# Optimization experiments

Measured on AMD Instinct MI355X. Metric: run time of the kernel, lower is better.

The kernel has to match this reference:

```python
import jax, jax.numpy as jnp
import numpy as np

N = 50000   # nodes
E = 800000  # edges (before self-loops)
B = 2       # extra batch dim
EPS = 1e-5  # BatchNorm eps


def _glorot(k, fi, fo):
    return jax.random.normal(k, (fi, fo), jnp.float32) * (1.0 / np.sqrt(fi))


def setup_inputs() -> dict:
    key = jax.random.key(0)
    ks = jax.random.split(key, 8)
    x = jax.random.normal(ks[0], (1, B, N, 216), jnp.float32)
    edge_index = jax.random.randint(ks[1], (2, E), 0, N, dtype=jnp.int64)
    return {
        "x": x,
        "W1": _glorot(ks[2], 216, 64), "b1": jnp.zeros((64,), jnp.float32),
        "g1": jnp.ones((64,), jnp.float32), "be1": jnp.zeros((64,), jnp.float32),
        "W2": _glorot(ks[3], 64, 8), "b2": jnp.zeros((8,), jnp.float32),
        "g2": jnp.ones((8,), jnp.float32), "be2": jnp.zeros((8,), jnp.float32),
        "W3": _glorot(ks[4], 8, 3), "b3": jnp.zeros((3,), jnp.float32),
        "edge_index": edge_index,
    }


def _gcn_norm(edge_index, n):
    # add self-loops, symmetric normalization D^-1/2 (A+I) D^-1/2
    loops = jnp.arange(n, dtype=edge_index.dtype)
    row = jnp.concatenate([edge_index[0], loops])
    col = jnp.concatenate([edge_index[1], loops])
    deg = jnp.zeros((n,), jnp.float32).at[col].add(1.0)
    dinv = jnp.where(deg > 0, jax.lax.rsqrt(deg), 0.0)
    norm = dinv[row] * dinv[col]  # [E+N]
    return row, col, norm


def _gcn(x, W, b, row, col, norm):
    # x: [1, B, N, Fin]; transform then propagate along node axis (-2)
    xw = jnp.einsum('ubnf,fo->ubno', x, W)
    msgs = xw[:, :, row, :] * norm[None, None, :, None]     # gather at sources
    out = jnp.zeros_like(xw).at[:, :, col, :].add(msgs)     # scatter to targets
    return out + b


def _bn(h, g, be):
    # h: [B, C, N]; batch statistics over (B, N) per channel (training mode)
    mean = h.mean(axis=(0, 2), keepdims=True)
    var = h.var(axis=(0, 2), keepdims=True)
    return (h - mean) * jax.lax.rsqrt(var + EPS) * g[None, :, None] + be[None, :, None]


def reference(x, W1, b1, g1, be1, W2, b2, g2, be2, W3, b3, edge_index):
    n = x.shape[-2]
    row, col, norm = _gcn_norm(edge_index, n)

    h = jax.nn.relu(_gcn(x, W1, b1, row, col, norm))        # [1,B,N,64]
    h = jnp.swapaxes(h[0], 1, 2)                            # [B,64,N]
    h = _bn(h, g1, be1)
    h = jnp.swapaxes(h, 1, 2)[None]                         # [1,B,N,64]

    x1 = _gcn(h, W2, b2, row, col, norm)                    # [1,B,N,8]
    x2 = jax.nn.relu(x1)
    x2 = jnp.swapaxes(x2[0], 1, 2)                          # [B,8,N]
    x2 = _bn(x2, g2, be2)
    x2 = jnp.swapaxes(x2, 1, 2)[None]                       # [1,B,N,8]

    out = _gcn(x2, W3, b3, row, col, norm)                  # [1,B,N,3]
    return (out, x1)
```

## Files before the change

kernel.cpp:

```cpp
#include <hip/hip_runtime.h>
#include <stdint.h>

#define N_NODES 50000
#define N_EDGES 800000
#define BB 2
#define F0 216
#define ROWS (BB*N_NODES)
#define BN_EPS 1e-5f
#define NSB 49


__global__ void k_count(const int* __restrict__ ei, int* __restrict__ cnt) {
    int e = blockIdx.x*blockDim.x + threadIdx.x;
    if (e < N_EDGES) {
        int c = ei[N_EDGES + e];
        atomicAdd(&cnt[c], 1);
    }
}

__global__ void k_dinv(const int* __restrict__ cnt, float* __restrict__ dinv) {
    int i = blockIdx.x*blockDim.x + threadIdx.x;
    if (i < N_NODES) dinv[i] = rsqrtf((float)(cnt[i] + 1));
}

__global__ void k_scanA(const int* __restrict__ cnt, int* __restrict__ incl, int* __restrict__ part) {
    __shared__ int s[1024];
    int t = threadIdx.x;
    int i = blockIdx.x*1024 + t;
    s[t] = (i < N_NODES) ? cnt[i] : 0;
    __syncthreads();
    for (int off=1; off<1024; off<<=1) {
        int a = (t >= off) ? s[t-off] : 0;
        __syncthreads();
        s[t] += a;
        __syncthreads();
    }
    if (i < N_NODES) incl[i] = s[t];
    if (t == 1023) part[blockIdx.x] = s[t];
}

__global__ void k_scanB(int* part) {
    if (threadIdx.x == 0 && blockIdx.x == 0) {
        int run = 0;
        for (int b=0; b<NSB; b++) { int v = part[b]; part[b] = run; run += v; }
    }
}

__global__ void k_scanC(const int* __restrict__ cnt, const int* __restrict__ incl, const int* __restrict__ part,
                        int* __restrict__ offs, int* __restrict__ cursor) {
    int i = blockIdx.x*1024 + threadIdx.x;
    if (i < N_NODES) {
        int inc = part[blockIdx.x] + incl[i];
        int ex = inc - cnt[i];
        offs[i] = ex; cursor[i] = ex;
        if (i == N_NODES-1) offs[N_NODES] = inc;
    }
}

__global__ void k_fill(const int* __restrict__ ei, const float* __restrict__ dinv,
                       int* __restrict__ cursor, int* __restrict__ csr_src, float* __restrict__ csr_w) {
    int e = blockIdx.x*blockDim.x + threadIdx.x;
    if (e < N_EDGES) {
        int r = ei[e];
        int c = ei[N_EDGES + e];
        int slot = atomicAdd(&cursor[c], 1);
        csr_src[slot] = r;
        csr_w[slot]  = dinv[r];
    }
}

#define KC 24
__global__ __launch_bounds__(256,2) void k_gemm1(const float* __restrict__ x, const float* __restrict__ W1,
                                                 float* __restrict__ xw) {
    __shared__ float xs[F0*64];
    int t = threadIdx.x;
    int row0 = blockIdx.x * 64;

    int r  = t & 63;
    int kg = t >> 6;
    bool rowok = (row0 + r) < ROWS;
    const float* xr = x + (size_t)(row0 + r) * F0;
    for (int kb = 0; kb < F0; kb += 16) {
        int k0 = kb + kg*4;
        if (k0 < F0) {
            float4 v; v.x=v.y=v.z=v.w=0.f;
            if (rowok) v = *reinterpret_cast<const float4*>(xr + k0);
            xs[(k0+0)*64 + r] = v.x;
            xs[(k0+1)*64 + r] = v.y;
            xs[(k0+2)*64 + r] = v.z;
            xs[(k0+3)*64 + r] = v.w;
        }
    }
    __syncthreads();

    int o2 = t & 31;
    int rg = t >> 5;
    float acc0[8], acc1[8];
    #pragma unroll
    for (int j=0;j<8;j++){ acc0[j]=0.f; acc1[j]=0.f; }

    for (int kc = 0; kc < F0; kc += KC) {
        float wa[KC], wb[KC];
        #pragma unroll
        for (int kk=0; kk<KC; kk++) {
            wa[kk] = W1[(kc+kk)*64 + o2];
            wb[kk] = W1[(kc+kk)*64 + o2 + 32];
        }
        #pragma unroll
        for (int kk=0; kk<KC; kk++) {
            const float* xk = xs + (kc+kk)*64 + rg*8;
            float4 x0 = *reinterpret_cast<const float4*>(xk);
            float4 x1 = *reinterpret_cast<const float4*>(xk + 4);
            float w0 = wa[kk], w1 = wb[kk];
            acc0[0] += x0.x*w0; acc0[1] += x0.y*w0; acc0[2] += x0.z*w0; acc0[3] += x0.w*w0;
            acc0[4] += x1.x*w0; acc0[5] += x1.y*w0; acc0[6] += x1.z*w0; acc0[7] += x1.w*w0;
            acc1[0] += x0.x*w1; acc1[1] += x0.y*w1; acc1[2] += x0.z*w1; acc1[3] += x0.w*w1;
            acc1[4] += x1.x*w1; acc1[5] += x1.y*w1; acc1[6] += x1.z*w1; acc1[7] += x1.w*w1;
        }
    }

    #pragma unroll
    for (int j=0;j<8;j++) {
        int grow = row0 + rg*8 + j;
        if (grow < ROWS) {
            xw[(size_t)grow*64 + o2]      = acc0[j];
            xw[(size_t)grow*64 + o2 + 32] = acc1[j];
        }
    }
}

__global__ __launch_bounds__(256) void k_prop1(const float* __restrict__ xw, const int* __restrict__ offs,
                       const int* __restrict__ csr_src, const float* __restrict__ csr_w,
                       const float* __restrict__ dinv, const float* __restrict__ b1,
                       float* __restrict__ h, float* __restrict__ stat) {
    __shared__ float lsum[64], lsq[64];
    int t = threadIdx.x;
    if (t < 64) { lsum[t]=0.f; lsq[t]=0.f; }
    __syncthreads();
    int f = t & 63;
    int wid = blockIdx.x*4 + (t>>6);
    int nwaves = gridDim.x*4;
    float bias = b1[f];
    float ls=0.f, lq=0.f;
    for (int d = wid; d < N_NODES; d += nwaves) {
        int s0 = offs[d], s1 = offs[d+1];
        float a0=0.f, a1=0.f, p0=0.f, p1=0.f, q0=0.f, q1=0.f, r0=0.f, r1=0.f;
        int e = s0;
        for (; e+4 <= s1; e += 4) {
            int i0=csr_src[e], i1=csr_src[e+1], i2=csr_src[e+2], i3=csr_src[e+3];
            float w0=csr_w[e], w1=csr_w[e+1], w2=csr_w[e+2], w3=csr_w[e+3];
            a0 += w0*xw[(size_t)i0*64+f];  a1 += w0*xw[(size_t)(N_NODES+i0)*64+f];
            p0 += w1*xw[(size_t)i1*64+f];  p1 += w1*xw[(size_t)(N_NODES+i1)*64+f];
            q0 += w2*xw[(size_t)i2*64+f];  q1 += w2*xw[(size_t)(N_NODES+i2)*64+f];
            r0 += w3*xw[(size_t)i3*64+f];  r1 += w3*xw[(size_t)(N_NODES+i3)*64+f];
        }
        for (; e < s1; e++) {
            int src = csr_src[e]; float w = csr_w[e];
            a0 += w*xw[(size_t)src*64+f];  a1 += w*xw[(size_t)(N_NODES+src)*64+f];
        }
        a0 += p0 + q0 + r0;
        a1 += p1 + q1 + r1;
        float sd = dinv[d];
        a0 += sd * xw[(size_t)d*64 + f];
        a1 += sd * xw[(size_t)(N_NODES+d)*64 + f];
        float h0 = fmaxf(sd*a0 + bias, 0.f);
        float h1 = fmaxf(sd*a1 + bias, 0.f);
        h[(size_t)d*64 + f] = h0;
        h[(size_t)(N_NODES+d)*64 + f] = h1;
        ls += h0 + h1;
        lq += h0*h0 + h1*h1;
    }
    atomicAdd(&lsum[f], ls);
    atomicAdd(&lsq[f], lq);
    __syncthreads();
    if (t < 64) {
        atomicAdd(&stat[t],     lsum[t]);
        atomicAdd(&stat[64+t],  lsq[t]);
    }
}

__global__ void k_bnfin(const float* __restrict__ stat, const float* __restrict__ g,
                        const float* __restrict__ be, float* __restrict__ sc, int C) {
    int f = threadIdx.x;
    if (f < C) {
        float inv_n = 1.0f / (float)(BB*N_NODES);
        float mean = stat[f]*inv_n;
        float var  = stat[C+f]*inv_n - mean*mean;
        float is   = rsqrtf(var + BN_EPS);
        float scale = g[f]*is;
        sc[f]   = scale;
        sc[C+f] = be[f] - mean*scale;
    }
}

__global__ __launch_bounds__(256) void k_bn1_gemm2(const float* __restrict__ h, const float* __restrict__ sc1,
                        const float* __restrict__ W2, float* __restrict__ t2) {
    __shared__ float hs[32][68];
    __shared__ float w2s[64*8];
    int t = threadIdx.x;
    for (int i=t; i<512; i+=256) w2s[i] = W2[i];
    int row0 = blockIdx.x*32;
    for (int idx=t; idx<2048; idx+=256) {
        int r = idx>>6, f = idx&63;
        int grow = row0 + r;
        hs[r][f] = (grow < ROWS) ? h[(size_t)grow*64+f]*sc1[f] + sc1[64+f] : 0.f;
    }
    __syncthreads();
    int r = t >> 3, o = t & 7;
    float acc = 0.f;
    #pragma unroll
    for (int f=0; f<64; f++) acc += hs[r][f] * w2s[f*8+o];
    int grow = row0 + r;
    if (grow < ROWS) t2[(size_t)grow*8 + o] = acc;
}

__global__ __launch_bounds__(256) void k_prop2(const float* __restrict__ t2, const int* __restrict__ offs,
                       const int* __restrict__ csr_src, const float* __restrict__ csr_w,
                       const float* __restrict__ dinv, const float* __restrict__ b2,
                       float* __restrict__ x1_out, float* __restrict__ stat) {
    __shared__ float lsum[8], lsq[8];
    int t = threadIdx.x;
    if (t < 8) { lsum[t]=0.f; lsq[t]=0.f; }
    __syncthreads();
    int lane = t & 63;
    int o = lane & 7, b = (lane>>3)&1, es = lane>>4;
    int wid = blockIdx.x*4 + (t>>6);
    int nwaves = gridDim.x*4;
    float bias = b2[o];
    float ls=0.f, lq=0.f;
    for (int d=wid; d<N_NODES; d+=nwaves) {
        int s0=offs[d], s1=offs[d+1];
        float accA=0.f, accB=0.f;
        int e = s0 + es;
        for (; e+4 < s1; e += 8) {
            accA += csr_w[e]   * t2[(size_t)(b*N_NODES+csr_src[e])*8 + o];
            accB += csr_w[e+4] * t2[(size_t)(b*N_NODES+csr_src[e+4])*8 + o];
        }
        if (e < s1) accA += csr_w[e] * t2[(size_t)(b*N_NODES+csr_src[e])*8 + o];
        float acc = accA + accB;
        acc += __shfl_xor(acc, 16, 64);
        acc += __shfl_xor(acc, 32, 64);
        float sd = dinv[d];
        float val = sd*(acc + sd*t2[(size_t)(b*N_NODES+d)*8 + o]) + bias;
        if (es == 0) {
            x1_out[(size_t)(b*N_NODES+d)*8 + o] = val;
            float rv = fmaxf(val, 0.f);
            ls += rv; lq += rv*rv;
        }
    }
    if (es == 0) { atomicAdd(&lsum[o], ls); atomicAdd(&lsq[o], lq); }
    __syncthreads();
    if (t < 8) { atomicAdd(&stat[t], lsum[t]); atomicAdd(&stat[8+t], lsq[t]); }
}

__global__ void k_bn2_gemm3(const float* __restrict__ x1, const float* __restrict__ sc2,
                            const float* __restrict__ W3, float* __restrict__ t3) {
    int rowi = blockIdx.x*blockDim.x + threadIdx.x;
    if (rowi < ROWS) {
        float v[8];
        #pragma unroll
        for (int o=0;o<8;o++) {
            float r = fmaxf(x1[(size_t)rowi*8+o], 0.f);
            v[o] = r*sc2[o] + sc2[8+o];
        }
        #pragma unroll
        for (int c=0;c<3;c++) {
            float acc=0.f;
            #pragma unroll
            for (int o=0;o<8;o++) acc += v[o]*W3[o*3+c];
            t3[(size_t)rowi*4+c] = acc;
        }
        t3[(size_t)rowi*4+3] = 0.f;
    }
}

__global__ __launch_bounds__(256) void k_prop3(const float* __restrict__ t3, const int* __restrict__ offs,
                       const int* __restrict__ csr_src, const float* __restrict__ csr_w,
                       const float* __restrict__ dinv, const float* __restrict__ b3,
                       float* __restrict__ outp) {
    int t = threadIdx.x;
    int lane = t & 63;
    int c = lane & 3, b = (lane>>2)&1, es = lane>>3;
    int wid = blockIdx.x*4 + (t>>6);
    int nwaves = gridDim.x*4;
    float bias = (c<3) ? b3[c] : 0.f;
    for (int d=wid; d<N_NODES; d+=nwaves) {
        int s0=offs[d], s1=offs[d+1];
        float accA=0.f, accB=0.f;
        int e = s0 + es;
        for (; e+8 < s1; e += 16) {
            accA += csr_w[e]   * t3[(size_t)(b*N_NODES+csr_src[e])*4 + c];
            accB += csr_w[e+8] * t3[(size_t)(b*N_NODES+csr_src[e+8])*4 + c];
        }
        if (e < s1) accA += csr_w[e] * t3[(size_t)(b*N_NODES+csr_src[e])*4 + c];
        float acc = accA + accB;
        acc += __shfl_xor(acc, 8, 64);
        acc += __shfl_xor(acc, 16, 64);
        acc += __shfl_xor(acc, 32, 64);
        float sd = dinv[d];
        float val = sd*(acc + sd*t3[(size_t)(b*N_NODES+d)*4 + c]) + bias;
        if (es == 0 && c < 3) outp[(size_t)(b*N_NODES+d)*3 + c] = val;
    }
}

static inline size_t align256(size_t x){ return (x + 255) & ~(size_t)255; }

extern "C" void kernel_launch(void* const* d_in, const int* in_sizes, int n_in,
                              void* d_out, int out_size, void* d_ws, size_t ws_size,
                              hipStream_t stream) {
    const float* x   = (const float*)d_in[0];
    const float* W1  = (const float*)d_in[1];
    const float* b1  = (const float*)d_in[2];
    const float* g1  = (const float*)d_in[3];
    const float* be1 = (const float*)d_in[4];
    const float* W2  = (const float*)d_in[5];
    const float* b2  = (const float*)d_in[6];
    const float* g2  = (const float*)d_in[7];
    const float* be2 = (const float*)d_in[8];
    const float* W3  = (const float*)d_in[9];
    const float* b3  = (const float*)d_in[10];
    const int*   ei  = (const int*)d_in[11];

    float* outp   = (float*)d_out;
    float* x1_out = (float*)d_out + BB*N_NODES*3;

    char* w = (char*)d_ws;
    size_t off = 0;
    auto alloc = [&](size_t bytes) { void* p = w + off; off = align256(off + bytes); return p; };
    int*   cnt    = (int*)  alloc(N_NODES*4);
    float* stat1  = (float*)alloc(128*4);
    float* stat2  = (float*)alloc(16*4);
    size_t zero_bytes = off;
    float* dinv   = (float*)alloc(N_NODES*4);
    int*   incl   = (int*)  alloc(N_NODES*4);
    int*   part   = (int*)  alloc(64*4);
    int*   offs   = (int*)  alloc((N_NODES+1)*4);
    int*   cursor = (int*)  alloc(N_NODES*4);
    int*   csr_src= (int*)  alloc((size_t)N_EDGES*4);
    float* csr_w  = (float*)alloc((size_t)N_EDGES*4);
    float* xw     = (float*)alloc((size_t)ROWS*64*4);
    float* h      = (float*)alloc((size_t)ROWS*64*4);
    float* sc1    = (float*)alloc(128*4);
    float* sc2    = (float*)alloc(16*4);
    float* t2     = xw;
    float* t3     = h;
    (void)ws_size; (void)in_sizes; (void)n_in; (void)out_size;

    hipMemsetAsync(d_ws, 0, zero_bytes, stream);

    k_count <<<(N_EDGES+255)/256, 256, 0, stream>>>(ei, cnt);
    k_dinv  <<<(N_NODES+255)/256, 256, 0, stream>>>(cnt, dinv);
    k_scanA <<<NSB, 1024, 0, stream>>>(cnt, incl, part);
    k_scanB <<<1, 64, 0, stream>>>(part);
    k_scanC <<<NSB, 1024, 0, stream>>>(cnt, incl, part, offs, cursor);
    k_fill  <<<(N_EDGES+255)/256, 256, 0, stream>>>(ei, dinv, cursor, csr_src, csr_w);

    k_gemm1 <<<(ROWS+63)/64, 256, 0, stream>>>(x, W1, xw);
    k_prop1 <<<2048, 256, 0, stream>>>(xw, offs, csr_src, csr_w, dinv, b1, h, stat1);
    k_bnfin <<<1, 64, 0, stream>>>(stat1, g1, be1, sc1, 64);
    k_bn1_gemm2 <<<(ROWS+31)/32, 256, 0, stream>>>(h, sc1, W2, t2);
    k_prop2 <<<2048, 256, 0, stream>>>(t2, offs, csr_src, csr_w, dinv, b2, x1_out, stat2);
    k_bnfin <<<1, 64, 0, stream>>>(stat2, g2, be2, sc2, 8);
    k_bn2_gemm3 <<<(ROWS+255)/256, 256, 0, stream>>>(x1_out, sc2, W3, t3);
    k_prop3 <<<2048, 256, 0, stream>>>(t3, offs, csr_src, csr_w, dinv, b3, outp);
}
```

Before: 514.5 us.

## Fuse small kernels, retile gemm1 row-major, unroll prop1 by eight, double prop grids

Folds the dinv computation into the scan kernel and the BN finalize into the consuming gemm kernels, removing three small launches. gemm1 now loads 32-row tiles contiguously with float4 copies into row-major shared memory, at four blocks per CU instead of two. prop1 gains an 8-way unrolled edge loop, and all propagation kernels launch 4096 blocks instead of 2048. The costs are redundant BN-stat math in every block/thread, gemm1 dropping its row-bound checks (valid only because ROWS divides by 32), and possible LDS bank conflicts in the row-major layout.

After: 609.7 us. +18.5%, slower.

```diff
diff --git a/kernel.cpp b/kernel.cpp
--- a/kernel.cpp
+++ b/kernel.cpp
@@ -8,6 +8,8 @@
 #define ROWS (BB*N_NODES)
 #define BN_EPS 1e-5f
 #define NSB 49
+#define KC 24
+#define TM 32
 
 
 __global__ void k_count(const int* __restrict__ ei, int* __restrict__ cnt) {
@@ -18,16 +20,14 @@
     }
 }
 
-__global__ void k_dinv(const int* __restrict__ cnt, float* __restrict__ dinv) {
-    int i = blockIdx.x*blockDim.x + threadIdx.x;
-    if (i < N_NODES) dinv[i] = rsqrtf((float)(cnt[i] + 1));
-}
-
-__global__ void k_scanA(const int* __restrict__ cnt, int* __restrict__ incl, int* __restrict__ part) {
+__global__ void k_scanA(const int* __restrict__ cnt, int* __restrict__ incl, int* __restrict__ part,
+                        float* __restrict__ dinv) {
     __shared__ int s[1024];
     int t = threadIdx.x;
     int i = blockIdx.x*1024 + t;
-    s[t] = (i < N_NODES) ? cnt[i] : 0;
+    int c = (i < N_NODES) ? cnt[i] : 0;
+    if (i < N_NODES) dinv[i] = rsqrtf((float)(c + 1));
+    s[t] = c;
     __syncthreads();
     for (int off=1; off<1024; off<<=1) {
         int a = (t >= off) ? s[t-off] : 0;
@@ -69,63 +69,50 @@
     }
 }
 
-#define KC 24
-__global__ __launch_bounds__(256,2) void k_gemm1(const float* __restrict__ x, const float* __restrict__ W1,
+__global__ __launch_bounds__(256,4) void k_gemm1(const float* __restrict__ x, const float* __restrict__ W1,
                                                  float* __restrict__ xw) {
-    __shared__ float xs[F0*64];
-    int t = threadIdx.x;
-    int row0 = blockIdx.x * 64;
-
-    int r  = t & 63;
-    int kg = t >> 6;
-    bool rowok = (row0 + r) < ROWS;
-    const float* xr = x + (size_t)(row0 + r) * F0;
-    for (int kb = 0; kb < F0; kb += 16) {
-        int k0 = kb + kg*4;
-        if (k0 < F0) {
-            float4 v; v.x=v.y=v.z=v.w=0.f;
-            if (rowok) v = *reinterpret_cast<const float4*>(xr + k0);
-            xs[(k0+0)*64 + r] = v.x;
-            xs[(k0+1)*64 + r] = v.y;
-            xs[(k0+2)*64 + r] = v.z;
-            xs[(k0+3)*64 + r] = v.w;
-        }
+    __shared__ float xs[TM*F0];
+    int t = threadIdx.x;
+    int row0 = blockIdx.x * TM;
+
+    const float4* xg = reinterpret_cast<const float4*>(x + (size_t)row0 * F0);
+    float4* xs4 = reinterpret_cast<float4*>(xs);
+    #pragma unroll
+    for (int i = 0; i < 7; i++) {
+        int idx = t + i*256;
+        if (idx < (TM*F0)/4) xs4[idx] = xg[idx];
     }
     __syncthreads();
 
     int o2 = t & 31;
-    int rg = t >> 5;
-    float acc0[8], acc1[8];
-    #pragma unroll
-    for (int j=0;j<8;j++){ acc0[j]=0.f; acc1[j]=0.f; }
+    int rw = t >> 5;
+    float acc0[4] = {0.f,0.f,0.f,0.f};
+    float acc1[4] = {0.f,0.f,0.f,0.f};
 
     for (int kc = 0; kc < F0; kc += KC) {
         float wa[KC], wb[KC];
         #pragma unroll
-        for (int kk=0; kk<KC; kk++) {
+        for (int kk = 0; kk < KC; kk++) {
             wa[kk] = W1[(kc+kk)*64 + o2];
             wb[kk] = W1[(kc+kk)*64 + o2 + 32];
         }
         #pragma unroll
-        for (int kk=0; kk<KC; kk++) {
-            const float* xk = xs + (kc+kk)*64 + rg*8;
-            float4 x0 = *reinterpret_cast<const float4*>(xk);
-            float4 x1 = *reinterpret_cast<const float4*>(xk + 4);
-            float w0 = wa[kk], w1 = wb[kk];
-            acc0[0] += x0.x*w0; acc0[1] += x0.y*w0; acc0[2] += x0.z*w0; acc0[3] += x0.w*w0;
-            acc0[4] += x1.x*w0; acc0[5] += x1.y*w0; acc0[6] += x1.z*w0; acc0[7] += x1.w*w0;
-            acc1[0] += x0.x*w1; acc1[1] += x0.y*w1; acc1[2] += x0.z*w1; acc1[3] += x0.w*w1;
-            acc1[4] += x1.x*w1; acc1[5] += x1.y*w1; acc1[6] += x1.z*w1; acc1[7] += x1.w*w1;
+        for (int j = 0; j < 4; j++) {
+            const float* xr = xs + (rw*4 + j)*F0 + kc;
+            #pragma unroll
+            for (int kq = 0; kq < KC/4; kq++) {
+                float4 xv = *reinterpret_cast<const float4*>(xr + 4*kq);
+                acc0[j] += xv.x*wa[4*kq] + xv.y*wa[4*kq+1] + xv.z*wa[4*kq+2] + xv.w*wa[4*kq+3];
+                acc1[j] += xv.x*wb[4*kq] + xv.y*wb[4*kq+1] + xv.z*wb[4*kq+2] + xv.w*wb[4*kq+3];
+            }
         }
     }
 
     #pragma unroll
-    for (int j=0;j<8;j++) {
-        int grow = row0 + rg*8 + j;
-        if (grow < ROWS) {
-            xw[(size_t)grow*64 + o2]      = acc0[j];
-            xw[(size_t)grow*64 + o2 + 32] = acc1[j];
-        }
+    for (int j = 0; j < 4; j++) {
+        int grow = row0 + rw*4 + j;
+        xw[(size_t)grow*64 + o2]      = acc0[j];
+        xw[(size_t)grow*64 + o2 + 32] = acc1[j];
     }
 }
 
@@ -146,6 +133,20 @@
         int s0 = offs[d], s1 = offs[d+1];
         float a0=0.f, a1=0.f, p0=0.f, p1=0.f, q0=0.f, q1=0.f, r0=0.f, r1=0.f;
         int e = s0;
+        for (; e+8 <= s1; e += 8) {
+            int i0=csr_src[e],   i1=csr_src[e+1], i2=csr_src[e+2], i3=csr_src[e+3];
+            int i4=csr_src[e+4], i5=csr_src[e+5], i6=csr_src[e+6], i7=csr_src[e+7];
+            float w0=csr_w[e],   w1=csr_w[e+1], w2=csr_w[e+2], w3=csr_w[e+3];
+            float w4=csr_w[e+4], w5=csr_w[e+5], w6=csr_w[e+6], w7=csr_w[e+7];
+            a0 += w0*xw[(size_t)i0*64+f];  a1 += w0*xw[(size_t)(N_NODES+i0)*64+f];
+            p0 += w1*xw[(size_t)i1*64+f];  p1 += w1*xw[(size_t)(N_NODES+i1)*64+f];
+            q0 += w2*xw[(size_t)i2*64+f];  q1 += w2*xw[(size_t)(N_NODES+i2)*64+f];
+            r0 += w3*xw[(size_t)i3*64+f];  r1 += w3*xw[(size_t)(N_NODES+i3)*64+f];
+            a0 += w4*xw[(size_t)i4*64+f];  a1 += w4*xw[(size_t)(N_NODES+i4)*64+f];
+            p0 += w5*xw[(size_t)i5*64+f];  p1 += w5*xw[(size_t)(N_NODES+i5)*64+f];
+            q0 += w6*xw[(size_t)i6*64+f];  q1 += w6*xw[(size_t)(N_NODES+i6)*64+f];
+            r0 += w7*xw[(size_t)i7*64+f];  r1 += w7*xw[(size_t)(N_NODES+i7)*64+f];
+        }
         for (; e+4 <= s1; e += 4) {
             int i0=csr_src[e], i1=csr_src[e+1], i2=csr_src[e+2], i3=csr_src[e+3];
             float w0=csr_w[e], w1=csr_w[e+1], w2=csr_w[e+2], w3=csr_w[e+3];
@@ -179,31 +180,29 @@
     }
 }
 
-__global__ void k_bnfin(const float* __restrict__ stat, const float* __restrict__ g,
-                        const float* __restrict__ be, float* __restrict__ sc, int C) {
-    int f = threadIdx.x;
-    if (f < C) {
-        float inv_n = 1.0f / (float)(BB*N_NODES);
-        float mean = stat[f]*inv_n;
-        float var  = stat[C+f]*inv_n - mean*mean;
-        float is   = rsqrtf(var + BN_EPS);
-        float scale = g[f]*is;
-        sc[f]   = scale;
-        sc[C+f] = be[f] - mean*scale;
-    }
-}
-
-__global__ __launch_bounds__(256) void k_bn1_gemm2(const float* __restrict__ h, const float* __restrict__ sc1,
+__global__ __launch_bounds__(256) void k_bn1_gemm2(const float* __restrict__ h, const float* __restrict__ stat,
+                        const float* __restrict__ g, const float* __restrict__ be,
                         const float* __restrict__ W2, float* __restrict__ t2) {
     __shared__ float hs[32][68];
     __shared__ float w2s[64*8];
-    int t = threadIdx.x;
+    __shared__ float scS[64], shS[64];
+    int t = threadIdx.x;
+    if (t < 64) {
+        float inv_n = 1.0f / (float)(BB*N_NODES);
+        float mean = stat[t]*inv_n;
+        float var  = stat[64+t]*inv_n - mean*mean;
+        float is   = rsqrtf(var + BN_EPS);
+        float scale = g[t]*is;
+        scS[t] = scale;
+        shS[t] = be[t] - mean*scale;
+    }
     for (int i=t; i<512; i+=256) w2s[i] = W2[i];
+    __syncthreads();
     int row0 = blockIdx.x*32;
     for (int idx=t; idx<2048; idx+=256) {
         int r = idx>>6, f = idx&63;
         int grow = row0 + r;
-        hs[r][f] = (grow < ROWS) ? h[(size_t)grow*64+f]*sc1[f] + sc1[64+f] : 0.f;
+        hs[r][f] = (grow < ROWS) ? h[(size_t)grow*64+f]*scS[f] + shS[f] : 0.f;
     }
     __syncthreads();
     int r = t >> 3, o = t & 7;
@@ -253,15 +252,22 @@
     if (t < 8) { atomicAdd(&stat[t], lsum[t]); atomicAdd(&stat[8+t], lsq[t]); }
 }
 
-__global__ void k_bn2_gemm3(const float* __restrict__ x1, const float* __restrict__ sc2,
+__global__ void k_bn2_gemm3(const float* __restrict__ x1, const float* __restrict__ stat,
+                            const float* __restrict__ g, const float* __restrict__ be,
                             const float* __restrict__ W3, float* __restrict__ t3) {
     int rowi = blockIdx.x*blockDim.x + threadIdx.x;
     if (rowi < ROWS) {
+        float inv_n = 1.0f / (float)(BB*N_NODES);
         float v[8];
         #pragma unroll
         for (int o=0;o<8;o++) {
+            float mean = stat[o]*inv_n;
+            float var  = stat[8+o]*inv_n - mean*mean;
+            float is   = rsqrtf(var + BN_EPS);
+            float scale = g[o]*is;
+            float shift = be[o] - mean*scale;
             float r = fmaxf(x1[(size_t)rowi*8+o], 0.f);
-            v[o] = r*sc2[o] + sc2[8+o];
+            v[o] = r*scale + shift;
         }
         #pragma unroll
         for (int c=0;c<3;c++) {
@@ -340,8 +346,6 @@
     float* csr_w  = (float*)alloc((size_t)N_EDGES*4);
     float* xw     = (float*)alloc((size_t)ROWS*64*4);
     float* h      = (float*)alloc((size_t)ROWS*64*4);
-    float* sc1    = (float*)alloc(128*4);
-    float* sc2    = (float*)alloc(16*4);
     float* t2     = xw;
     float* t3     = h;
     (void)ws_size; (void)in_sizes; (void)n_in; (void)out_size;
@@ -349,18 +353,15 @@
     hipMemsetAsync(d_ws, 0, zero_bytes, stream);
 
     k_count <<<(N_EDGES+255)/256, 256, 0, stream>>>(ei, cnt);
-    k_dinv  <<<(N_NODES+255)/256, 256, 0, stream>>>(cnt, dinv);
-    k_scanA <<<NSB, 1024, 0, stream>>>(cnt, incl, part);
+    k_scanA <<<NSB, 1024, 0, stream>>>(cnt, incl, part, dinv);
     k_scanB <<<1, 64, 0, stream>>>(part);
     k_scanC <<<NSB, 1024, 0, stream>>>(cnt, incl, part, offs, cursor);
     k_fill  <<<(N_EDGES+255)/256, 256, 0, stream>>>(ei, dinv, cursor, csr_src, csr_w);
 
-    k_gemm1 <<<(ROWS+63)/64, 256, 0, stream>>>(x, W1, xw);
-    k_prop1 <<<2048, 256, 0, stream>>>(xw, offs, csr_src, csr_w, dinv, b1, h, stat1);
-    k_bnfin <<<1, 64, 0, stream>>>(stat1, g1, be1, sc1, 64);
-    k_bn1_gemm2 <<<(ROWS+31)/32, 256, 0, stream>>>(h, sc1, W2, t2);
-    k_prop2 <<<2048, 256, 0, stream>>>(t2, offs, csr_src, csr_w, dinv, b2, x1_out, stat2);
-    k_bnfin <<<1, 64, 0, stream>>>(stat2, g2, be2, sc2, 8);
-    k_bn2_gemm3 <<<(ROWS+255)/256, 256, 0, stream>>>(x1_out, sc2, W3, t3);
-    k_prop3 <<<2048, 256, 0, stream>>>(t3, offs, csr_src, csr_w, dinv, b3, outp);
-}
+    k_gemm1 <<<ROWS/TM, 256, 0, stream>>>(x, W1, xw);
+    k_prop1 <<<4096, 256, 0, stream>>>(xw, offs, csr_src, csr_w, dinv, b1, h, stat1);
+    k_bn1_gemm2 <<<(ROWS+31)/32, 256, 0, stream>>>(h, stat1, g1, be1, W2, t2);
+    k_prop2 <<<4096, 256, 0, stream>>>(t2, offs, csr_src, csr_w, dinv, b2, x1_out, stat2);
+    k_bn2_gemm3 <<<(ROWS+255)/256, 256, 0, stream>>>(x1_out, stat2, g2, be2, W3, t3);
+    k_prop3 <<<4096, 256, 0, stream>>>(t3, offs, csr_src, csr_w, dinv, b3, outp);
+}
```
